# Performance work log

Hardware: AMD Instinct MI355X
Metric: run time of the kernel (lower is better)

The kernel has to match this reference:

```python
import jax, jax.numpy as jnp
import numpy as np

DENSE_W = 0.7  # unused in learned fusion path but kept for parity
SPARSE_W = 0.3

def _l2norm(x):
    return x / jnp.linalg.norm(x, axis=-1, keepdims=True)

def setup_inputs() -> dict:
    key = jax.random.key(0)
    ks = jax.random.split(key, 8)
    Q, D, dim = 32, 4096, 384
    feat = 2 * dim + 2  # 770
    query_dense = _l2norm(jax.random.normal(ks[0], (Q, dim), jnp.float32))
    doc_dense = _l2norm(jax.random.normal(ks[1], (D, dim), jnp.float32))
    sparse_scores = jax.random.uniform(ks[2], (Q, D), jnp.float32)
    W1 = jax.random.normal(ks[3], (feat, 384), jnp.float32) * (1.0 / np.sqrt(feat))
    b1 = jnp.zeros((384,), jnp.float32)
    W2 = jax.random.normal(ks[4], (384, 192), jnp.float32) * (1.0 / np.sqrt(384))
    b2 = jnp.zeros((192,), jnp.float32)
    W3 = jax.random.normal(ks[5], (192, 1), jnp.float32) * (1.0 / np.sqrt(192))
    b3 = jnp.zeros((1,), jnp.float32)
    return {"query_dense": query_dense, "doc_dense": doc_dense,
            "sparse_scores": sparse_scores,
            "W1": W1, "b1": b1, "W2": W2, "b2": b2, "W3": W3, "b3": b3}

def reference(query_dense, doc_dense, sparse_scores, W1, b1, W2, b2, W3, b3):
    # dense cosine similarity (inputs are L2-normalized): [Q, D]
    dense_scores = query_dense @ doc_dense.T
    Q, D = dense_scores.shape
    dim = query_dense.shape[1]
    # Vectorized equivalent of the per-pair gather+concat double loop:
    # feature[q, d] = [query_dense[q], doc_dense[d], dense[q,d], sparse[q,d]]
    qf = jnp.broadcast_to(query_dense[:, None, :], (Q, D, dim))
    df = jnp.broadcast_to(doc_dense[None, :, :], (Q, D, dim))
    features = jnp.concatenate(
        [qf, df, dense_scores[..., None], sparse_scores[..., None]], axis=-1)  # [Q, D, 2*dim+2]
    # 4-layer fusion MLP (Dropout is identity at inference)
    h = jax.nn.relu(features @ W1 + b1)
    h = jax.nn.relu(h @ W2 + b2)
    fusion_weights = jax.nn.sigmoid((h @ W3 + b3)[..., 0])  # [Q, D]
    final_scores = fusion_weights * dense_scores + (1.0 - fusion_weights) * sparse_scores
    return final_scores, dense_scores, sparse_scores
```

## Files before the change

### kernel.cpp

```cpp
#include <hip/hip_runtime.h>
#include <hip/hip_bf16.h>

typedef __attribute__((ext_vector_type(2)))  float f32x2;
typedef __attribute__((ext_vector_type(4)))  float f32x4;
typedef __attribute__((ext_vector_type(16))) float f32x16;
typedef __attribute__((ext_vector_type(8)))  short bf16x8;
typedef __attribute__((ext_vector_type(4)))  unsigned int u32x4;

__device__ __forceinline__ short f2bf(float x){
    __hip_bfloat16 h = __float2bfloat16(x);
    return __builtin_bit_cast(short, h);
}
__device__ __forceinline__ float bf2f(short x){
    unsigned int u = ((unsigned int)(unsigned short)x) << 16;
    return __builtin_bit_cast(float, u);
}
__device__ __forceinline__ unsigned int cvt2(float lo, float hi){
    unsigned int r;
    asm("v_cvt_pk_bf16_f32 %0, %1, %2" : "=v"(r) : "v"(lo), "v"(hi));
    return r;
}

__global__ __launch_bounds__(256)
void pre_kernel(const float* __restrict__ query, const float* __restrict__ doc,
                const float* __restrict__ sparse, const float* __restrict__ W1,
                const float* __restrict__ b1, const float* __restrict__ W2,
                float* __restrict__ out_dense, float* __restrict__ out_sparse,
                short* __restrict__ Bws, float* __restrict__ Aq,
                float* __restrict__ W1cdf, short* __restrict__ W2t){
    __shared__ float ldsq[32*388];
    __shared__ float ldsd[16*388];
    const int b = blockIdx.x, tid = threadIdx.x;

    if (b < 256){
        const int d0 = b*16;
        #pragma unroll
        for (int i=0;i<12;i++){ int idx = tid + i*256; int row = idx/96, c4 = idx%96;
            *(f32x4*)(ldsq + row*388 + c4*4) = *(const f32x4*)(query + row*384 + c4*4); }
        #pragma unroll
        for (int i=0;i<6;i++){ int idx = tid + i*256; int row = idx/96, c4 = idx%96;
            *(f32x4*)(ldsd + row*388 + c4*4) = *(const f32x4*)(doc + (d0+row)*384 + c4*4); }
        __syncthreads();
        const int q = tid>>3, dg = tid&7;
        const f32x4* q4  = (const f32x4*)(ldsq + q*388);
        const f32x4* d4a = (const f32x4*)(ldsd + dg*388);
        const f32x4* d4b = (const f32x4*)(ldsd + (dg+8)*388);
        f32x4 s0 = {0.f,0.f,0.f,0.f}, s1 = {0.f,0.f,0.f,0.f};
        #pragma unroll 4
        for (int k=0;k<96;k++){
            const f32x4 qv = q4[k];
            s0 += qv*d4a[k];
            s1 += qv*d4b[k];
        }
        out_dense[q*4096 + d0 + dg]     = s0[0]+s0[1]+s0[2]+s0[3];
        out_dense[q*4096 + d0 + dg + 8] = s1[0]+s1[1]+s1[2]+s1[3];
        if (tid < 128){
            int qq = tid>>2, c4 = tid&3;
            *(f32x4*)(out_sparse + qq*4096 + d0 + c4*4) = *(const f32x4*)(sparse + qq*4096 + d0 + c4*4);
        }
    } else if (b < 514){
        const int bb = b - 256;
        const int w = tid >> 6, lane = tid & 63;
        const int cl = lane & 15, quad = lane >> 4;
        const float* src; const float* wrow; int r0; bool isA;
        if (bb < 256){ r0 = bb*16;       src = doc;   wrow = W1 + 384*384; isA = false; }
        else         { r0 = (bb-256)*16; src = query; wrow = W1;           isA = true;  }

        f32x4 acc[6];
        #pragma unroll
        for (int t=0;t<6;t++) acc[t] = (f32x4){0.f,0.f,0.f,0.f};

        #pragma unroll 1
        for (int s=0;s<12;s++){
            const float* ap = src + (r0+cl)*384 + s*32 + quad*8;
            const f32x4 a0 = *(const f32x4*)ap;
            const f32x4 a1 = *(const f32x4*)(ap+4);
            bf16x8 af;
            #pragma unroll
            for (int j=0;j<4;j++){ af[j] = f2bf(a0[j]); af[4+j] = f2bf(a1[j]); }
            const float* wk = wrow + (s*32 + quad*8)*384;
            #pragma unroll
            for (int tt=0;tt<6;tt++){
                const int col = (w*6+tt)*16 + cl;
                bf16x8 bf_;
                #pragma unroll
                for (int j=0;j<8;j++) bf_[j] = f2bf(wk[j*384 + col]);
                acc[tt] = __builtin_amdgcn_mfma_f32_16x16x32_bf16(af, bf_, acc[tt], 0, 0, 0);
            }
        }
        #pragma unroll
        for (int tt=0;tt<6;tt++){
            const int col = (w*6+tt)*16 + cl;
            if (isA){
                const float b1v = b1[col];
                #pragma unroll
                for (int r=0;r<4;r++)
                    Aq[(r0 + quad*4 + r)*384 + col] = acc[tt][r] + b1v;
            } else {
                #pragma unroll
                for (int r=0;r<4;r++)
                    Bws[(r0 + quad*4 + r)*384 + col] = f2bf(acc[tt][r]);
            }
        }
    } else if (b == 514){
        #pragma unroll
        for (int i=0;i<3;i++){
            int o = tid + i*256;
            W1cdf[o] = (o < 384) ? W1[768*384 + o] : W1[769*384 + (o - 384)];
        }
    } else {
        const int t0 = (b - 515)*256 + tid;
        #pragma unroll
        for (int i=0;i<9;i++){
            int c = t0 + i*1024;
            int lane_c = c & 63, st = c >> 6;
            int s = st/6, t2 = st%6;
            int n = t2*32 + (lane_c&31), kb = s*16 + ((lane_c>>5)&1)*8;
            bf16x8 v;
            #pragma unroll
            for (int j=0;j<8;j++) v[j] = f2bf(W2[(kb+j)*192 + n]);
            *(bf16x8*)(W2t + c*8) = v;
        }
    }
}

#define STEP(BW,A0,A1,S) do{                                                        \
    const int kf_ = (S)*16 + kbase;                                                 \
    const f32x4 wcA = *(const f32x4*)(lcd + kf_);                                   \
    const f32x4 wcB = *(const f32x4*)(lcd + kf_ + 4);                               \
    const f32x4 wdA = *(const f32x4*)(lcd + 384 + kf_);                             \
    const f32x4 wdB = *(const f32x4*)(lcd + 384 + kf_ + 4);                         \
    const short* lp_ = lw + ((S)*384 + lane)*8;                                     \
    const bf16x8 bfr0 = *(const bf16x8*)(lp_);                                      \
    const bf16x8 bfr1 = *(const bf16x8*)(lp_ + 512);                                \
    const bf16x8 bfr2 = *(const bf16x8*)(lp_ + 1024);                               \
    const bf16x8 bfr3 = *(const bf16x8*)(lp_ + 1536);                               \
    const bf16x8 bfr4 = *(const bf16x8*)(lp_ + 2048);                               \
    const bf16x8 bfr5 = *(const bf16x8*)(lp_ + 2560);                               \
    u32x4 frw_;                                                                     \
    { f32x2 h = {A0[0] + bf2f(BW[0]), A0[1] + bf2f(BW[1])};                         \
      h += dsv2 * (f32x2){wcA[0],wcA[1]}; h += ssv2 * (f32x2){wdA[0],wdA[1]};       \
      frw_[0] = cvt2(fmaxf(h[0],0.f), fmaxf(h[1],0.f)); }                           \
    { f32x2 h = {A0[2] + bf2f(BW[2]), A0[3] + bf2f(BW[3])};                         \
      h += dsv2 * (f32x2){wcA[2],wcA[3]}; h += ssv2 * (f32x2){wdA[2],wdA[3]};       \
      frw_[1] = cvt2(fmaxf(h[0],0.f), fmaxf(h[1],0.f)); }                           \
    { f32x2 h = {A1[0] + bf2f(BW[4]), A1[1] + bf2f(BW[5])};                         \
      h += dsv2 * (f32x2){wcB[0],wcB[1]}; h += ssv2 * (f32x2){wdB[0],wdB[1]};       \
      frw_[2] = cvt2(fmaxf(h[0],0.f), fmaxf(h[1],0.f)); }                           \
    { f32x2 h = {A1[2] + bf2f(BW[6]), A1[3] + bf2f(BW[7])};                         \
      h += dsv2 * (f32x2){wcB[2],wcB[3]}; h += ssv2 * (f32x2){wdB[2],wdB[3]};       \
      frw_[3] = cvt2(fmaxf(h[0],0.f), fmaxf(h[1],0.f)); }                           \
    const bf16x8 fr_ = __builtin_bit_cast(bf16x8, frw_);                            \
    acc[0] = __builtin_amdgcn_mfma_f32_32x32x16_bf16(fr_, bfr0, acc[0], 0, 0, 0);   \
    acc[1] = __builtin_amdgcn_mfma_f32_32x32x16_bf16(fr_, bfr1, acc[1], 0, 0, 0);   \
    acc[2] = __builtin_amdgcn_mfma_f32_32x32x16_bf16(fr_, bfr2, acc[2], 0, 0, 0);   \
    acc[3] = __builtin_amdgcn_mfma_f32_32x32x16_bf16(fr_, bfr3, acc[3], 0, 0, 0);   \
    acc[4] = __builtin_amdgcn_mfma_f32_32x32x16_bf16(fr_, bfr4, acc[4], 0, 0, 0);   \
    acc[5] = __builtin_amdgcn_mfma_f32_32x32x16_bf16(fr_, bfr5, acc[5], 0, 0, 0);   \
  }while(0)

__global__ __launch_bounds__(512, 2)
void main_kernel(const float* __restrict__ Aq, const short* __restrict__ Bws,
                 const float* __restrict__ W1cdf, const short* __restrict__ W2t,
                 const float* __restrict__ b2, const float* __restrict__ W3,
                 const float* __restrict__ b3, const float* __restrict__ sparse,
                 const float* __restrict__ dense_in, float* __restrict__ out_final){
    __shared__ __align__(16) short lw[73728];
    __shared__ __align__(16) float lcd[768];
    const int tid = threadIdx.x;

    #pragma unroll
    for (int i=0;i<18;i++){
        int c = tid + i*512;
        *(f32x4*)(lw + c*8) = *(const f32x4*)(W2t + c*8);
    }
    if (tid < 192)
        *(f32x4*)(lcd + tid*4) = *(const f32x4*)(W1cdf + tid*4);
    __syncthreads();

    const int lane = tid & 63, w = tid >> 6;
    const int m = lane & 31, q2 = lane >> 5;
    const int kbase = q2*8;
    const float b3v = b3[0];
    const int dcol0 = blockIdx.x*16 + w;

    const float dsv0 = dense_in[m*4096 + dcol0];
    const float ssv0 = sparse[m*4096 + dcol0];
    const float dsv1 = dense_in[m*4096 + dcol0 + 8];
    const float ssv1 = sparse[m*4096 + dcol0 + 8];

    #pragma unroll 1
    for (int t4=0; t4<2; t4++){
        const int dcol = dcol0 + t4*8;
        const float dsv = t4 ? dsv1 : dsv0;
        const float ssv = t4 ? ssv1 : ssv0;
        const f32x2 dsv2 = {dsv, dsv}, ssv2 = {ssv, ssv};

        f32x16 acc[6];
        #pragma unroll
        for (int t=0;t<6;t++)
            #pragma unroll
            for (int r=0;r<16;r++) acc[t][r] = 0.0f;

        const short* bp = Bws + dcol*384;
        const float* ap = Aq + m*384;

        bf16x8 bwA = *(const bf16x8*)(bp + kbase);
        f32x4  aA0 = *(const f32x4*)(ap + kbase);
        f32x4  aA1 = *(const f32x4*)(ap + kbase + 4);
        bf16x8 bwB = *(const bf16x8*)(bp + 16 + kbase);
        f32x4  aB0 = *(const f32x4*)(ap + 16 + kbase);
        f32x4  aB1 = *(const f32x4*)(ap + 16 + kbase + 4);
        bf16x8 bwC = *(const bf16x8*)(bp + 32 + kbase);
        f32x4  aC0 = *(const f32x4*)(ap + 32 + kbase);
        f32x4  aC1 = *(const f32x4*)(ap + 32 + kbase + 4);

        #pragma unroll 1
        for (int s=0; s<24; s+=3){
            STEP(bwA, aA0, aA1, s);
            { const int kp = (s+3 < 24) ? (s+3)*16 + kbase : kbase;
              bwA = *(const bf16x8*)(bp + kp);
              aA0 = *(const f32x4*)(ap + kp);
              aA1 = *(const f32x4*)(ap + kp + 4); }
            STEP(bwB, aB0, aB1, s+1);
            { const int kp = (s+4 < 24) ? (s+4)*16 + kbase : kbase;
              bwB = *(const bf16x8*)(bp + kp);
              aB0 = *(const f32x4*)(ap + kp);
              aB1 = *(const f32x4*)(ap + kp + 4); }
            STEP(bwC, aC0, aC1, s+2);
            { const int kp = (s+5 < 24) ? (s+5)*16 + kbase : kbase;
              bwC = *(const bf16x8*)(bp + kp);
              aC0 = *(const f32x4*)(ap + kp);
              aC1 = *(const f32x4*)(ap + kp + 4); }
        }

        float p[16];
        #pragma unroll
        for (int r=0;r<16;r++) p[r] = 0.0f;
        #pragma unroll
        for (int t=0;t<6;t++){
            const int n = t*32 + m;
            const float b2v = b2[n];
            const float w3v = W3[n];
            #pragma unroll
            for (int r=0;r<16;r++)
                p[r] += fmaxf(acc[t][r] + b2v, 0.0f) * w3v;
        }
        #pragma unroll
        for (int mask=1; mask<32; mask<<=1){
            #pragma unroll
            for (int r=0;r<16;r++) p[r] += __shfl_xor(p[r], mask);
        }
        float myp = p[0];
        #pragma unroll
        for (int r=1;r<16;r++) myp = (m==r) ? p[r] : myp;
        if (m < 16){
            const int row = (m&3) + 8*(m>>2) + 4*q2;
            float logit = myp + b3v;
            float wgt = 1.0f/(1.0f + __expf(-logit));
            float dd = dense_in[row*4096 + dcol];
            float ss = sparse[row*4096 + dcol];
            out_final[row*4096 + dcol] = wgt*dd + (1.0f - wgt)*ss;
        }
    }
}

extern "C" void kernel_launch(void* const* d_in, const int* in_sizes, int n_in,
                              void* d_out, int out_size, void* d_ws, size_t ws_size,
                              hipStream_t stream){
    const float* query  = (const float*)d_in[0];
    const float* doc    = (const float*)d_in[1];
    const float* sparse = (const float*)d_in[2];
    const float* W1     = (const float*)d_in[3];
    const float* b1     = (const float*)d_in[4];
    const float* W2     = (const float*)d_in[5];
    const float* b2     = (const float*)d_in[6];
    const float* W3     = (const float*)d_in[7];
    const float* b3     = (const float*)d_in[8];

    float* out_final  = (float*)d_out;
    float* out_dense  = (float*)d_out + 131072;
    float* out_sparse = (float*)d_out + 262144;

    short* Bws   = (short*)d_ws;
    float* Aq    = (float*)((char*)d_ws + 3145728);
    float* W1cdf = (float*)((char*)d_ws + 3194880);
    short* W2t   = (short*)((char*)d_ws + 3197952);

    hipLaunchKernelGGL(pre_kernel,  dim3(519), dim3(256), 0, stream,
                       query, doc, sparse, W1, b1, W2, out_dense, out_sparse, Bws, Aq, W1cdf, W2t);
    hipLaunchKernelGGL(main_kernel, dim3(256), dim3(512), 0, stream,
                       Aq, Bws, W1cdf, W2t, b2, W3, b3, sparse, out_dense, out_final);
}
```

Measured before the change: 128.2 us.

## Split W1 projection into a bf16 pre-conversion pass and a prefetched MFMA GEMM kernel

The doc/query projection through W1 previously converted fp32 to bf16 inline, using strided scalar loads of W1 inside the MFMA loop. It is now split into two kernels. The first converts W1 into an MFMA-fragment-ordered bf16 layout and converts doc and query to bf16. The second runs the GEMM with contiguous 16-byte fragment loads, double-buffered one k-step ahead. This adds a kernel launch and extra workspace traffic in exchange for cheaper, coalesced loads in the GEMM.

```diff
diff --git a/kernel.cpp b/kernel.cpp
--- a/kernel.cpp
+++ b/kernel.cpp
@@ -5,6 +5,7 @@
 typedef __attribute__((ext_vector_type(4)))  float f32x4;
 typedef __attribute__((ext_vector_type(16))) float f32x16;
 typedef __attribute__((ext_vector_type(8)))  short bf16x8;
+typedef __attribute__((ext_vector_type(2)))  unsigned int u32x2;
 typedef __attribute__((ext_vector_type(4)))  unsigned int u32x4;
 
 __device__ __forceinline__ short f2bf(float x){
@@ -22,12 +23,12 @@
 }
 
 __global__ __launch_bounds__(256)
-void pre_kernel(const float* __restrict__ query, const float* __restrict__ doc,
-                const float* __restrict__ sparse, const float* __restrict__ W1,
-                const float* __restrict__ b1, const float* __restrict__ W2,
-                float* __restrict__ out_dense, float* __restrict__ out_sparse,
-                short* __restrict__ Bws, float* __restrict__ Aq,
-                float* __restrict__ W1cdf, short* __restrict__ W2t){
+void pre0_kernel(const float* __restrict__ query, const float* __restrict__ doc,
+                 const float* __restrict__ sparse, const float* __restrict__ W1,
+                 const float* __restrict__ W2,
+                 float* __restrict__ out_dense, float* __restrict__ out_sparse,
+                 short* __restrict__ W1t, short* __restrict__ docb, short* __restrict__ qb16,
+                 float* __restrict__ W1cdf, short* __restrict__ W2t){
     __shared__ float ldsq[32*388];
     __shared__ float ldsd[16*388];
     const int b = blockIdx.x, tid = threadIdx.x;
@@ -58,58 +59,50 @@
             int qq = tid>>2, c4 = tid&3;
             *(f32x4*)(out_sparse + qq*4096 + d0 + c4*4) = *(const f32x4*)(sparse + qq*4096 + d0 + c4*4);
         }
-    } else if (b < 514){
-        const int bb = b - 256;
-        const int w = tid >> 6, lane = tid & 63;
-        const int cl = lane & 15, quad = lane >> 4;
-        const float* src; const float* wrow; int r0; bool isA;
-        if (bb < 256){ r0 = bb*16;       src = doc;   wrow = W1 + 384*384; isA = false; }
-        else         { r0 = (bb-256)*16; src = query; wrow = W1;           isA = true;  }
-
-        f32x4 acc[6];
-        #pragma unroll
-        for (int t=0;t<6;t++) acc[t] = (f32x4){0.f,0.f,0.f,0.f};
-
-        #pragma unroll 1
-        for (int s=0;s<12;s++){
-            const float* ap = src + (r0+cl)*384 + s*32 + quad*8;
-            const f32x4 a0 = *(const f32x4*)ap;
-            const f32x4 a1 = *(const f32x4*)(ap+4);
-            bf16x8 af;
-            #pragma unroll
-            for (int j=0;j<4;j++){ af[j] = f2bf(a0[j]); af[4+j] = f2bf(a1[j]); }
-            const float* wk = wrow + (s*32 + quad*8)*384;
-            #pragma unroll
-            for (int tt=0;tt<6;tt++){
-                const int col = (w*6+tt)*16 + cl;
-                bf16x8 bf_;
-                #pragma unroll
-                for (int j=0;j<8;j++) bf_[j] = f2bf(wk[j*384 + col]);
-                acc[tt] = __builtin_amdgcn_mfma_f32_16x16x32_bf16(af, bf_, acc[tt], 0, 0, 0);
-            }
-        }
-        #pragma unroll
-        for (int tt=0;tt<6;tt++){
-            const int col = (w*6+tt)*16 + cl;
-            if (isA){
-                const float b1v = b1[col];
-                #pragma unroll
-                for (int r=0;r<4;r++)
-                    Aq[(r0 + quad*4 + r)*384 + col] = acc[tt][r] + b1v;
-            } else {
-                #pragma unroll
-                for (int r=0;r<4;r++)
-                    Bws[(r0 + quad*4 + r)*384 + col] = f2bf(acc[tt][r]);
-            }
-        }
-    } else if (b == 514){
+    } else if (b < 328){
+        const int lt0 = (b-256)*256 + tid;
+        #pragma unroll
+        for (int i=0;i<2;i++){
+            const int lt    = lt0 + i*18432;
+            const int chunk = lt >> 6, lane = lt & 63;
+            const int cl = lane & 15, quad = lane >> 4;
+            const int half = (chunk >= 288) ? 1 : 0;
+            const int cs = chunk - half*288;
+            const int s = cs/24, ct = cs%24;
+            const float* src = W1 + (half*384 + s*32 + quad*8)*384 + ct*16 + cl;
+            float v[8];
+            #pragma unroll
+            for (int j=0;j<8;j++) v[j] = src[j*384];
+            u32x4 o;
+            o[0] = cvt2(v[0],v[1]); o[1] = cvt2(v[2],v[3]);
+            o[2] = cvt2(v[4],v[5]); o[3] = cvt2(v[6],v[7]);
+            *(u32x4*)(W1t + chunk*512 + lane*8) = o;
+        }
+    } else if (b < 424){
+        const int t0 = (b-328)*256 + tid;
+        #pragma unroll
+        for (int i=0;i<16;i++){
+            const int g = t0 + i*24576;
+            const f32x4 v = *(const f32x4*)(doc + g*4);
+            u32x2 o; o[0] = cvt2(v[0],v[1]); o[1] = cvt2(v[2],v[3]);
+            *(u32x2*)(docb + g*4) = o;
+        }
+    } else if (b == 424){
+        #pragma unroll
+        for (int i=0;i<12;i++){
+            const int g = tid + i*256;
+            const f32x4 v = *(const f32x4*)(query + g*4);
+            u32x2 o; o[0] = cvt2(v[0],v[1]); o[1] = cvt2(v[2],v[3]);
+            *(u32x2*)(qb16 + g*4) = o;
+        }
+    } else if (b == 425){
         #pragma unroll
         for (int i=0;i<3;i++){
             int o = tid + i*256;
             W1cdf[o] = (o < 384) ? W1[768*384 + o] : W1[769*384 + (o - 384)];
         }
     } else {
-        const int t0 = (b - 515)*256 + tid;
+        const int t0 = (b - 426)*256 + tid;
         #pragma unroll
         for (int i=0;i<9;i++){
             int c = t0 + i*1024;
@@ -120,6 +113,61 @@
             #pragma unroll
             for (int j=0;j<8;j++) v[j] = f2bf(W2[(kb+j)*192 + n]);
             *(bf16x8*)(W2t + c*8) = v;
+        }
+    }
+}
+
+__global__ __launch_bounds__(256)
+void pre1_kernel(const short* __restrict__ docb, const short* __restrict__ qb16,
+                 const short* __restrict__ W1t, const float* __restrict__ b1,
+                 short* __restrict__ Bws, float* __restrict__ Aq){
+    const int b = blockIdx.x, tid = threadIdx.x;
+    const int w = tid >> 6, lane = tid & 63;
+    const int cl = lane & 15, quad = lane >> 4;
+
+    const short* src; const short* wt; int r0; bool isA;
+    if (b < 256){ r0 = b*16;       src = docb; wt = W1t + 147456; isA = false; }
+    else        { r0 = (b-256)*16; src = qb16; wt = W1t;          isA = true;  }
+
+    const short* ap = src + (r0+cl)*384 + quad*8;
+    const short* wp = wt + (w*6)*512 + lane*8;
+
+    f32x4 acc[6];
+    #pragma unroll
+    for (int t=0;t<6;t++) acc[t] = (f32x4){0.f,0.f,0.f,0.f};
+
+    bf16x8 a_c = *(const bf16x8*)(ap);
+    bf16x8 b_c[6];
+    #pragma unroll
+    for (int tt=0;tt<6;tt++) b_c[tt] = *(const bf16x8*)(wp + tt*512);
+
+    #pragma unroll 1
+    for (int s=0;s<12;s++){
+        const int sn = (s < 11) ? s+1 : 0;
+        const bf16x8 a_n = *(const bf16x8*)(ap + sn*32);
+        bf16x8 b_n[6];
+        #pragma unroll
+        for (int tt=0;tt<6;tt++) b_n[tt] = *(const bf16x8*)(wp + sn*12288 + tt*512);
+        #pragma unroll
+        for (int tt=0;tt<6;tt++)
+            acc[tt] = __builtin_amdgcn_mfma_f32_16x16x32_bf16(a_c, b_c[tt], acc[tt], 0, 0, 0);
+        a_c = a_n;
+        #pragma unroll
+        for (int tt=0;tt<6;tt++) b_c[tt] = b_n[tt];
+    }
+
+    #pragma unroll
+    for (int tt=0;tt<6;tt++){
+        const int col = (w*6+tt)*16 + cl;
+        if (isA){
+            const float b1v = b1[col];
+            #pragma unroll
+            for (int r=0;r<4;r++)
+                Aq[(r0 + quad*4 + r)*384 + col] = acc[tt][r] + b1v;
+        } else {
+            #pragma unroll
+            for (int r=0;r<4;r++)
+                Bws[(r0 + quad*4 + r)*384 + col] = f2bf(acc[tt][r]);
         }
     }
 }
@@ -286,9 +334,15 @@
     float* Aq    = (float*)((char*)d_ws + 3145728);
     float* W1cdf = (float*)((char*)d_ws + 3194880);
     short* W2t   = (short*)((char*)d_ws + 3197952);
-
-    hipLaunchKernelGGL(pre_kernel,  dim3(519), dim3(256), 0, stream,
-                       query, doc, sparse, W1, b1, W2, out_dense, out_sparse, Bws, Aq, W1cdf, W2t);
+    short* W1t   = (short*)((char*)d_ws + 3345408);
+    short* docb  = (short*)((char*)d_ws + 3935232);
+    short* qb16  = (short*)((char*)d_ws + 7080960);
+
+    hipLaunchKernelGGL(pre0_kernel, dim3(430), dim3(256), 0, stream,
+                       query, doc, sparse, W1, W2, out_dense, out_sparse,
+                       W1t, docb, qb16, W1cdf, W2t);
+    hipLaunchKernelGGL(pre1_kernel, dim3(258), dim3(256), 0, stream,
+                       docb, qb16, W1t, b1, Bws, Aq);
     hipLaunchKernelGGL(main_kernel, dim3(256), dim3(512), 0, stream,
                        Aq, Bws, W1cdf, W2t, b2, W3, b3, sparse, out_dense, out_final);
 }
```

New measurement: 125.6 us. 1.02x faster.
